# Kernel optimization log

Measured on AMD Instinct MI355X. Metric: run time of the kernel, lower is better.

Reference implementation:

```python
import jax, jax.numpy as jnp
import numpy as np

B, S, D, H, DH, F = 2, 2048, 1024, 16, 64, 4096
EPS = 1e-5


def layernorm(x, gamma, beta):
    mu = jnp.mean(x, axis=-1, keepdims=True)
    var = jnp.mean((x - mu) ** 2, axis=-1, keepdims=True)
    return (x - mu) * jax.lax.rsqrt(var + EPS) * gamma + beta


def setup_inputs() -> dict:
    key = jax.random.key(0)
    ks = jax.random.split(key, 13)
    sc = 0.02
    return {
        "x": jax.random.normal(ks[0], (B, S, D), jnp.float32),
        "W_Q": jax.random.normal(ks[1], (H, DH, D), jnp.float32) * sc,  # per-head [d_head, d_model]
        "W_K": jax.random.normal(ks[2], (H, DH, D), jnp.float32) * sc,
        "W_V": jax.random.normal(ks[3], (H, DH, D), jnp.float32) * sc,
        "W_O": jax.random.normal(ks[4], (H * DH, D), jnp.float32) * sc,
        "W_up": jax.random.normal(ks[5], (D, F), jnp.float32) * sc,
        "b_up": jax.random.normal(ks[6], (F,), jnp.float32) * sc,
        "W_down": jax.random.normal(ks[7], (F, D), jnp.float32) * sc,
        "b_down": jax.random.normal(ks[8], (D,), jnp.float32) * sc,
        "gamma_1": jnp.ones((D,), jnp.float32),
        "beta_1": jnp.zeros((D,), jnp.float32),
        "gamma_2": jnp.ones((D,), jnp.float32),
        "beta_2": jnp.zeros((D,), jnp.float32),
    }


def reference(x, W_Q, W_K, W_V, W_O, W_up, b_up, W_down, b_down, gamma_1, beta_1, gamma_2, beta_2):
    u = layernorm(x, gamma_1, beta_1)
    # per-head projections: input @ W.t() -> [B, H, S, DH]
    Q = jnp.einsum("bsd,hed->bhse", u, W_Q)
    K = jnp.einsum("bsd,hed->bhse", u, W_K)
    V = jnp.einsum("bsd,hed->bhse", u, W_V)
    # Faithful quirk: original does K.reshape(B, DH, S) (raw reshape, NOT transpose)
    K_r = K.reshape(B, H, DH, S)
    scores = jnp.matmul(Q, K_r) / D  # [B,H,S,S]; quirk: scaled by d_model, not sqrt(d_head)
    attn = jax.nn.softmax(scores, axis=-1)
    heads = jnp.matmul(attn, V)  # [B,H,S,DH]
    heads_cat = heads.transpose(0, 2, 1, 3).reshape(B, S, H * DH)  # concat heads on last dim
    z1 = x + heads_cat @ W_O
    v1 = layernorm(z1, gamma_2, beta_2)
    v3 = jax.nn.gelu(v1 @ W_up + b_up, approximate=False)
    z2 = z1 + v3 @ W_down + b_down
    return z2
```

## Files before the change

kernel.cpp:

```cpp
#include <hip/hip_runtime.h>
#include <hip/hip_bf16.h>


typedef __attribute__((ext_vector_type(8))) short short8v;
typedef __attribute__((ext_vector_type(4))) short short4v;
typedef __attribute__((ext_vector_type(4))) float f32x4;

__device__ __forceinline__ float b2f(unsigned short u) {
    unsigned int x = ((unsigned int)u) << 16;
    float f;
    __builtin_memcpy(&f, &x, 4);
    return f;
}
__device__ __forceinline__ unsigned short f2b(float f) {
    unsigned int x;
    __builtin_memcpy(&x, &f, 4);
    unsigned int r = (x + 0x7FFFu + ((x >> 16) & 1u)) >> 16;
    return (unsigned short)r;
}
__device__ __forceinline__ void gload16(const unsigned short* g, unsigned short* l) {
    __builtin_amdgcn_global_load_lds(
        (const __attribute__((address_space(1))) unsigned int*)g,
        (__attribute__((address_space(3))) unsigned int*)l, 16, 0, 0);
}
__device__ __forceinline__ bool is_f32(const unsigned int* flagp) {
    return *flagp == 0x3F800000u;
}

__global__ __launch_bounds__(256) void cast_qkv_k(const void* __restrict__ s0,
                                                  const void* __restrict__ s1,
                                                  const void* __restrict__ s2,
                                                  unsigned short* __restrict__ dst,
                                                  const unsigned int* __restrict__ flagp) {
    const bool f32 = is_f32(flagp);
    const int seg = blockIdx.x >> 9;
    const int i = ((blockIdx.x & 511) * 256 + threadIdx.x) * 8;
    const void* src = seg == 0 ? s0 : (seg == 1 ? s1 : s2);
    unsigned short* d = dst + (size_t)seg * 1048576 + i;
    if (f32) {
        const float* s = (const float*)src + i;
        float4 a = *(const float4*)s;
        float4 b = *(const float4*)(s + 4);
        union { unsigned short u[8]; int4 v; } o;
        o.u[0] = f2b(a.x); o.u[1] = f2b(a.y); o.u[2] = f2b(a.z); o.u[3] = f2b(a.w);
        o.u[4] = f2b(b.x); o.u[5] = f2b(b.y); o.u[6] = f2b(b.z); o.u[7] = f2b(b.w);
        *(int4*)d = o.v;
    } else {
        *(int4*)d = *(const int4*)((const unsigned short*)src + i);
    }
}

__global__ __launch_bounds__(256) void cast_small_k(const void* __restrict__ s0,
                                                    const void* __restrict__ s1,
                                                    const void* __restrict__ s2,
                                                    const void* __restrict__ s3,
                                                    const void* __restrict__ s4,
                                                    const void* __restrict__ s5,
                                                    unsigned short* __restrict__ dst,
                                                    const unsigned int* __restrict__ flagp) {
    const bool f32 = is_f32(flagp);
    const int seg = blockIdx.x < 2 ? 0 : blockIdx.x - 1;
    const void* srcs[6] = {s0, s1, s2, s3, s4, s5};
    const int offs[6] = {0, 4096, 5120, 6144, 7168, 8192};
    const int lens[6] = {4096, 1024, 1024, 1024, 1024, 1024};
    const int base = (blockIdx.x < 2 ? blockIdx.x * 2048 : 0);
    const int i = base + threadIdx.x * 8;
    if (i >= lens[seg]) return;
    const void* src = srcs[seg];
    unsigned short* d = dst + offs[seg] + i;
    if (f32) {
        const float* s = (const float*)src + i;
        float4 a = *(const float4*)s;
        float4 b = *(const float4*)(s + 4);
        union { unsigned short u[8]; int4 v; } o;
        o.u[0] = f2b(a.x); o.u[1] = f2b(a.y); o.u[2] = f2b(a.z); o.u[3] = f2b(a.w);
        o.u[4] = f2b(b.x); o.u[5] = f2b(b.y); o.u[6] = f2b(b.z); o.u[7] = f2b(b.w);
        *(int4*)d = o.v;
    } else {
        *(int4*)d = *(const int4*)((const unsigned short*)src + i);
    }
}

__global__ __launch_bounds__(256) void castT_k(const void* __restrict__ src,
                                               unsigned short* __restrict__ dst,
                                               int rows, int cols,
                                               const unsigned int* __restrict__ flagp) {
    const bool f32 = is_f32(flagp);
    __shared__ float tile[32][33];
    const int t = threadIdx.x, tx = t & 31, ty = t >> 5;
    const int c0 = blockIdx.x * 32, r0 = blockIdx.y * 32;
#pragma unroll
    for (int i = 0; i < 4; i++) {
        int r = r0 + ty + i * 8;
        float v;
        if (f32) v = ((const float*)src)[(size_t)r * cols + c0 + tx];
        else     v = b2f(((const unsigned short*)src)[(size_t)r * cols + c0 + tx]);
        tile[ty + i * 8][tx] = v;
    }
    __syncthreads();
#pragma unroll
    for (int i = 0; i < 4; i++) {
        int c = c0 + ty + i * 8;
        dst[(size_t)c * rows + r0 + tx] = f2b(tile[tx][ty + i * 8]);
    }
}

__global__ __launch_bounds__(256) void kvT_k(const unsigned short* __restrict__ Kn,
                                             const unsigned short* __restrict__ Vn,
                                             unsigned short* __restrict__ Ktt,
                                             unsigned short* __restrict__ Vtt) {
    __shared__ unsigned short tile[64][72];
    const int blk = blockIdx.x;
    const int bh = blk >> 6;
    const int sub = blk & 63;
    const size_t base = (size_t)bh * (2048 * 64);
    const unsigned short* src;
    unsigned short* dst;
    int R, C, r0, c0;
    if (sub < 32) { src = Kn + base; dst = Ktt + base; R = 64;   C = 2048; r0 = 0;              c0 = sub * 64; }
    else          { src = Vn + base; dst = Vtt + base; R = 2048; C = 64;   r0 = (sub - 32) * 64; c0 = 0; }
    const int t = threadIdx.x;
    const int tx = t & 7, ty = t >> 3;
#pragma unroll
    for (int i = 0; i < 2; i++) {
        int r = ty + i * 32;
        union { int4 v; unsigned short u[8]; } ld;
        ld.v = *(const int4*)&src[(size_t)(r0 + r) * C + c0 + tx * 8];
#pragma unroll
        for (int k = 0; k < 8; k++) tile[tx * 8 + k][r] = ld.u[k];
    }
    __syncthreads();
#pragma unroll
    for (int i = 0; i < 2; i++) {
        int c = ty + i * 32;
        union { int4 v; unsigned short u[8]; } stv;
#pragma unroll
        for (int k = 0; k < 8; k++) stv.u[k] = tile[c][tx * 8 + k];
        *(int4*)&dst[(size_t)(c0 + c) * R + r0 + tx * 8] = stv.v;
    }
}

__global__ __launch_bounds__(256) void fin_k(const float* __restrict__ src,
                                             const unsigned short* __restrict__ P0,
                                             const unsigned short* __restrict__ P1,
                                             const unsigned short* __restrict__ P2,
                                             const unsigned short* __restrict__ P3,
                                             void* __restrict__ dst,
                                             const unsigned short* __restrict__ bias,
                                             const unsigned int* __restrict__ flagp) {
    const bool f32 = is_f32(flagp);
    const int i = (blockIdx.x * 256 + threadIdx.x) * 4;
    float4 v = *(const float4*)(src + i);
    uint2 p0 = *(const uint2*)(P0 + i);
    uint2 p1 = *(const uint2*)(P1 + i);
    uint2 p2 = *(const uint2*)(P2 + i);
    uint2 p3 = *(const uint2*)(P3 + i);
    int c = i & 1023;
    v.x += b2f(bias[c])     + b2f((unsigned short)(p0.x & 0xffff)) + b2f((unsigned short)(p1.x & 0xffff))
                            + b2f((unsigned short)(p2.x & 0xffff)) + b2f((unsigned short)(p3.x & 0xffff));
    v.y += b2f(bias[c + 1]) + b2f((unsigned short)(p0.x >> 16))    + b2f((unsigned short)(p1.x >> 16))
                            + b2f((unsigned short)(p2.x >> 16))    + b2f((unsigned short)(p3.x >> 16));
    v.z += b2f(bias[c + 2]) + b2f((unsigned short)(p0.y & 0xffff)) + b2f((unsigned short)(p1.y & 0xffff))
                            + b2f((unsigned short)(p2.y & 0xffff)) + b2f((unsigned short)(p3.y & 0xffff));
    v.w += b2f(bias[c + 3]) + b2f((unsigned short)(p0.y >> 16))    + b2f((unsigned short)(p1.y >> 16))
                            + b2f((unsigned short)(p2.y >> 16))    + b2f((unsigned short)(p3.y >> 16));
    if (f32) {
        *(float4*)((float*)dst + i) = v;
    } else {
        union { unsigned short u[4]; uint2 q; } o;
        o.u[0] = f2b(v.x); o.u[1] = f2b(v.y); o.u[2] = f2b(v.z); o.u[3] = f2b(v.w);
        *(uint2*)((unsigned short*)dst + i) = o.q;
    }
}

template <int MODE>
__global__ __launch_bounds__(256) void ln_k(const void* __restrict__ inp,
                                            unsigned short* __restrict__ outp,
                                            const unsigned short* __restrict__ gamma,
                                            const unsigned short* __restrict__ beta,
                                            const unsigned int* __restrict__ flagp) {
    const int row = blockIdx.x, t = threadIdx.x;
    float xv[4];
    bool f32 = (MODE == 1) ? true : is_f32(flagp);
    if (f32) {
        const float* p = (const float*)inp + (size_t)row * 1024 + t * 4;
        float4 v = *(const float4*)p;
        xv[0] = v.x; xv[1] = v.y; xv[2] = v.z; xv[3] = v.w;
    } else {
        const unsigned short* p = (const unsigned short*)inp + (size_t)row * 1024 + t * 4;
        uint2 v = *(const uint2*)p;
        xv[0] = b2f((unsigned short)(v.x & 0xffff));
        xv[1] = b2f((unsigned short)(v.x >> 16));
        xv[2] = b2f((unsigned short)(v.y & 0xffff));
        xv[3] = b2f((unsigned short)(v.y >> 16));
    }
    float s = xv[0] + xv[1] + xv[2] + xv[3];
    float q = xv[0] * xv[0] + xv[1] * xv[1] + xv[2] * xv[2] + xv[3] * xv[3];
#pragma unroll
    for (int off = 32; off >= 1; off >>= 1) {
        s += __shfl_xor(s, off);
        q += __shfl_xor(q, off);
    }
    __shared__ float ls[8];
    if ((t & 63) == 0) { ls[t >> 6] = s; ls[4 + (t >> 6)] = q; }
    __syncthreads();
    s = ls[0] + ls[1] + ls[2] + ls[3];
    q = ls[4] + ls[5] + ls[6] + ls[7];
    const float mu = s * (1.f / 1024.f);
    const float rs = rsqrtf(q * (1.f / 1024.f) - mu * mu + 1e-5f);
    union { unsigned short u[4]; uint2 v; } o;
#pragma unroll
    for (int i = 0; i < 4; i++) {
        int c = t * 4 + i;
        o.u[i] = f2b((xv[i] - mu) * rs * b2f(gamma[c]) + b2f(beta[c]));
    }
    *(uint2*)(outp + (size_t)row * 1024 + t * 4) = o.v;
}

template <int EPI>
__global__ __launch_bounds__(256) void gemm_k(const unsigned short* __restrict__ A,
                                              const unsigned short* __restrict__ Bm,
                                              unsigned short* __restrict__ C,
                                              unsigned short* __restrict__ C2,
                                              unsigned short* __restrict__ C3,
                                              const unsigned short* __restrict__ bias,
                                              float* __restrict__ outf,
                                              const void* __restrict__ xres,
                                              const unsigned int* __restrict__ flagp,
                                              int N, int ldk, int tilesM, int tilesN,
                                              int kLen) {
    __shared__ unsigned short As[2][128 * 32];
    __shared__ unsigned short Bs[2][128 * 32];
    const int t = threadIdx.x;
    const int w = t >> 6, lane = t & 63, ln = t & 15, quad = (t & 63) >> 4;
    const int wm = w >> 1, wn = w & 1;
    const int bm = blockIdx.x % tilesM;
    const int bn = (blockIdx.x / tilesM) % tilesN;
    const int kc = blockIdx.x / (tilesM * tilesN);
    const int m0 = bm << 7, n0 = bn << 7;
    const int k0 = kc * kLen;
    f32x4 acc[4][4] = {};

    const int srow = lane >> 2;
    const int scol = (lane & 3) << 3;

    const size_t arow[2] = {(size_t)(m0 + (0 * 4 + w) * 16 + srow) * ldk + scol,
                            (size_t)(m0 + (1 * 4 + w) * 16 + srow) * ldk + scol};
    const size_t brow[2] = {(size_t)(n0 + (0 * 4 + w) * 16 + srow) * ldk + scol,
                            (size_t)(n0 + (1 * 4 + w) * 16 + srow) * ldk + scol};

#pragma unroll
    for (int r = 0; r < 2; r++) {
        const int blk = r * 4 + w;
        gload16(&A[arow[r] + k0], &As[0][blk * 512]);
        gload16(&Bm[brow[r] + k0], &Bs[0][blk * 512]);
    }

    int cur = 0;
    for (int kt = k0; kt < k0 + kLen; kt += 32) {
        asm volatile("s_waitcnt vmcnt(0)" ::: "memory");
        __syncthreads();
        if (kt + 32 < k0 + kLen) {
#pragma unroll
            for (int r = 0; r < 2; r++) {
                const int blk = r * 4 + w;
                gload16(&A[arow[r] + kt + 32], &As[cur ^ 1][blk * 512]);
                gload16(&Bm[brow[r] + kt + 32], &Bs[cur ^ 1][blk * 512]);
            }
        }
        short8v af[4], bfv[4];
#pragma unroll
        for (int mi = 0; mi < 4; mi++)
            af[mi] = *(const short8v*)&As[cur][(wm * 64 + mi * 16 + ln) * 32 + quad * 8];
#pragma unroll
        for (int nj = 0; nj < 4; nj++)
            bfv[nj] = *(const short8v*)&Bs[cur][(wn * 64 + nj * 16 + ln) * 32 + quad * 8];
#pragma unroll
        for (int mi = 0; mi < 4; mi++)
#pragma unroll
            for (int nj = 0; nj < 4; nj++)
                acc[mi][nj] = __builtin_amdgcn_mfma_f32_16x16x32_bf16(
                    af[mi], bfv[nj], acc[mi][nj], 0, 0, 0);
        cur ^= 1;
    }

    bool xf32 = false;
    if (EPI == 3) xf32 = is_f32(flagp);

#pragma unroll
    for (int mi = 0; mi < 4; mi++) {
#pragma unroll
        for (int nj = 0; nj < 4; nj++) {
#pragma unroll
            for (int r = 0; r < 4; r++) {
                const int m = m0 + wm * 64 + mi * 16 + quad * 4 + r;
                const int n = n0 + wn * 64 + nj * 16 + ln;
                float v = acc[mi][nj][r];
                if (EPI == 3) {
                    float xv = xf32 ? ((const float*)xres)[(size_t)m * N + n]
                                    : b2f(((const unsigned short*)xres)[(size_t)m * N + n]);
                    outf[(size_t)m * N + n] = v + xv;
                }
            }
        }
    }
}

template <int EPI>
__global__ __launch_bounds__(512, 2) void gemm256_k(const unsigned short* __restrict__ A,
                                                    const unsigned short* __restrict__ Bm,
                                                    unsigned short* __restrict__ C,
                                                    unsigned short* __restrict__ C2,
                                                    unsigned short* __restrict__ C3,
                                                    const unsigned short* __restrict__ bias,
                                                    int N, int ldk, int tilesM, int tilesN,
                                                    int kLen) {
    __shared__ unsigned short As[4][8192];
    __shared__ unsigned short Bs[4][8192];
    const int t = threadIdx.x;
    const int w = t >> 6, l = t & 63, ln = t & 15, quad = (t & 63) >> 4;
    const int wm = w >> 2, wn = w & 3;

    const int nwg = gridDim.x;
    const int wg = ((int)blockIdx.x & 7) * (nwg >> 3) + ((int)blockIdx.x >> 3);

    const int bm = wg % tilesM;
    const int bn = (wg / tilesM) % tilesN;
    const int kc = wg / (tilesM * tilesN);
    const int m0 = bm << 8, n0 = bn << 8;
    const int k0 = kc * kLen;
    const int nk = kLen >> 5;

    const int lrow = l >> 2;
    const int lswz = (((l & 3) ^ (lrow & 3)) << 3);
    const size_t aG0 = (size_t)(m0 + (w << 4) + lrow) * ldk + k0 + lswz;
    const size_t aG1 = aG0 + ((size_t)ldk << 7);
    const size_t bG0 = (size_t)(n0 + (w << 4) + lrow) * ldk + k0 + lswz;
    const size_t bG1 = bG0 + ((size_t)ldk << 7);
    const int ldsLo = w * 512;
    const int ldsHi = 4096 + w * 512;

    const int swz8 = ((quad ^ (ln & 3)) << 3);
    const int raBase = (wm * 128 + ln) * 32 + swz8;
    const int rbBase = (wn * 64 + ln) * 32 + swz8;

    f32x4 acc[8][4] = {};

    gload16(&A[aG0], &As[0][ldsLo]);
    gload16(&Bm[bG0], &Bs[0][ldsLo]);
    gload16(&A[aG1], &As[0][ldsHi]);
    gload16(&Bm[bG1], &Bs[0][ldsHi]);
    if (nk > 1) {
        gload16(&A[aG0 + 32], &As[1][ldsLo]);
        gload16(&Bm[bG0 + 32], &Bs[1][ldsLo]);
        gload16(&A[aG1 + 32], &As[1][ldsHi]);
        gload16(&Bm[bG1 + 32], &Bs[1][ldsHi]);
    }

    for (int tI = 0; tI < nk; ++tI) {
        const int buf = tI & 3;
        if (tI + 1 < nk) {
            asm volatile("s_waitcnt vmcnt(4)" ::: "memory");
        } else {
            asm volatile("s_waitcnt vmcnt(0)" ::: "memory");
        }
        __builtin_amdgcn_s_barrier();
        __builtin_amdgcn_sched_barrier(0);

        const unsigned short* Ab = As[buf];
        const unsigned short* Bb = Bs[buf];
        const int nb = (tI + 2) & 3;
        const size_t ko = (size_t)(tI + 2) << 5;

        if (tI + 2 < nk) {
            gload16(&A[aG0 + ko], &As[nb][ldsLo]);
            gload16(&Bm[bG0 + ko], &Bs[nb][ldsLo]);
            gload16(&A[aG1 + ko], &As[nb][ldsHi]);
            gload16(&Bm[bG1 + ko], &Bs[nb][ldsHi]);
        }
        short8v bf[4], af[8];
#pragma unroll
        for (int nj = 0; nj < 4; nj++) bf[nj] = *(const short8v*)&Bb[rbBase + nj * 512];
#pragma unroll
        for (int mi = 0; mi < 8; mi++) af[mi] = *(const short8v*)&Ab[raBase + mi * 512];
        asm volatile("s_waitcnt lgkmcnt(0)" ::: "memory");
        __builtin_amdgcn_sched_barrier(0);
        __builtin_amdgcn_s_setprio(1);
#pragma unroll
        for (int mi = 0; mi < 8; mi++)
#pragma unroll
            for (int nj = 0; nj < 4; nj++)
                acc[mi][nj] = __builtin_amdgcn_mfma_f32_16x16x32_bf16(
                    af[mi], bf[nj], acc[mi][nj], 0, 0, 0);
        __builtin_amdgcn_s_setprio(0);
    }

    unsigned short* Cp = C;
    if (EPI == 8) Cp = (kc == 0) ? C : (kc == 1) ? (C + 4194304) : (kc == 2) ? C2 : C3;

#pragma unroll
    for (int mi = 0; mi < 8; mi++) {
#pragma unroll
        for (int nj = 0; nj < 4; nj++) {
#pragma unroll
            for (int r = 0; r < 4; r++) {
                const int m = m0 + wm * 128 + mi * 16 + quad * 4 + r;
                const int n = n0 + wn * 64 + nj * 16 + ln;
                float v = acc[mi][nj][r];
                if (EPI == 4) {
                    float x = v + b2f(bias[n]);
                    Cp[(size_t)m * N + n] = f2b(0.5f * x * (1.f + erff(x * 0.70710678118654752f)));
                } else if (EPI == 6) {
                    int b = m >> 11, s = m & 2047;
                    int seg = n >> 10, nn = n & 1023, h = nn >> 6, e = nn & 63;
                    size_t off = ((size_t)(b * 16 + h) * 2048 + s) * 64 + e;
                    if (seg == 0)      C[off]  = f2b(v);
                    else if (seg == 1) C2[off] = f2b(v);
                    else               C3[off] = f2b(v);
                } else {
                    Cp[(size_t)m * N + n] = f2b(v);
                }
            }
        }
    }
}

__global__ __launch_bounds__(512, 4) void attn_k(const unsigned short* __restrict__ Q,
                                                 const unsigned short* __restrict__ Kt,
                                                 const unsigned short* __restrict__ Vt,
                                                 unsigned short* __restrict__ Hd) {
    __shared__ unsigned short Ks[2][2][128 * 32];
    __shared__ unsigned short Vs[2][64 * 128];
    const int t = threadIdx.x;
    const int w = t >> 6, l = t & 63, ln = t & 15, quad = (t & 63) >> 4;
    const int qt = blockIdx.x & 15, bh = blockIdx.x >> 4;
    const int b = bh >> 4, h = bh & 15;
    const int i0 = qt << 7;

    short8v aq[2];
    {
        const unsigned short* qp =
            Q + ((size_t)bh * 2048 + i0 + w * 16 + ln) * 64 + quad * 8;
        aq[0] = *(const short8v*)qp;
        aq[1] = *(const short8v*)(qp + 32);
    }

    const size_t kbase = (size_t)bh * (2048 * 64);
    const size_t vbase = (size_t)bh * (64 * 2048);

    size_t ksrc[2]; int klds[2];
    size_t vsrc[2]; int vlds[2];
#pragma unroll
    for (int r = 0; r < 2; r++) {
        int idx2 = w * 2 + r;
        int ksp = idx2 & 1, J = idx2 >> 1;
        ksrc[r] = (size_t)(J * 16 + (l >> 2)) * 64 + ksp * 32 + (l & 3) * 8;
        klds[r] = ksp * 4096 + J * 512;
        int c = idx2;
        int e = c * 4 + (l >> 4), pp = l & 15;
        int g = (pp & 8) | ((pp & 7) ^ (e & 7));
        vsrc[r] = (size_t)e * 2048 + g * 8;
        vlds[r] = c * 512;
    }

#pragma unroll
    for (int r = 0; r < 2; r++) {
        gload16(Kt + kbase + ksrc[r], &Ks[0][0][0] + klds[r]);
        gload16(Vt + vbase + vsrc[r], &Vs[0][0] + vlds[r]);
    }

    f32x4 O[4] = {};
    float lsum = 0.f;
    int cur = 0;
    const float sc = 9.765625e-4f;

    for (int jt = 0; jt < 16; jt++) {
        asm volatile("s_waitcnt vmcnt(0)" ::: "memory");
        __syncthreads();
        if (jt < 15) {
            const size_t j1 = (size_t)(jt + 1) << 7;
#pragma unroll
            for (int r = 0; r < 2; r++) {
                gload16(Kt + kbase + j1 * 64 + ksrc[r], &Ks[cur ^ 1][0][0] + klds[r]);
                gload16(Vt + vbase + j1 + vsrc[r], &Vs[cur ^ 1][0] + vlds[r]);
            }
        }

        f32x4 S[8] = {};
#pragma unroll
        for (int ks = 0; ks < 2; ks++) {
#pragma unroll
            for (int nj = 0; nj < 8; nj++) {
                short8v bk = *(const short8v*)&Ks[cur][ks][(nj * 16 + ln) * 32 + quad * 8];
                S[nj] = __builtin_amdgcn_mfma_f32_16x16x32_bf16(bk, aq[ks], S[nj], 0, 0, 0);
            }
        }
        short4v pk[8];
#pragma unroll
        for (int nj = 0; nj < 8; nj++) {
            float p0 = __expf(S[nj][0] * sc);
            float p1 = __expf(S[nj][1] * sc);
            float p2 = __expf(S[nj][2] * sc);
            float p3 = __expf(S[nj][3] * sc);
            lsum += (p0 + p1) + (p2 + p3);
            union { unsigned int w2[2]; short4v v; } pu;
            asm("v_cvt_pk_bf16_f32 %0, %1, %2" : "=v"(pu.w2[0]) : "v"(p0), "v"(p1));
            asm("v_cvt_pk_bf16_f32 %0, %1, %2" : "=v"(pu.w2[1]) : "v"(p2), "v"(p3));
            pk[nj] = pu.v;
        }
#pragma unroll
        for (int nj = 0; nj < 8; nj++) {
            int g = 2 * nj + (quad >> 1);
            int pos = (g & 8) | ((g & 7) ^ (ln & 7));
            int off = pos * 8 + (quad & 1) * 4;
#pragma unroll
            for (int ne = 0; ne < 4; ne++) {
                short4v bv = *(const short4v*)&Vs[cur][(ne * 16 + ln) * 128 + off];
                O[ne] = __builtin_amdgcn_mfma_f32_16x16x16bf16_1k(pk[nj], bv, O[ne], 0, 0, 0);
            }
        }
        cur ^= 1;
    }

    lsum += __shfl_xor(lsum, 16);
    lsum += __shfl_xor(lsum, 32);

#pragma unroll
    for (int r = 0; r < 4; r++) {
        float lr = __shfl(lsum, quad * 4 + r);
        float inv = 1.f / lr;
#pragma unroll
        for (int ne = 0; ne < 4; ne++) {
            int i = i0 + w * 16 + quad * 4 + r;
            int e = ne * 16 + ln;
            Hd[((size_t)(b * 2048 + i)) * 1024 + h * 64 + e] = f2b(O[ne][r] * inv);
        }
    }
}

extern "C" void kernel_launch(void* const* d_in, const int* in_sizes, int n_in,
                              void* d_out, int out_size, void* d_ws, size_t ws_size,
                              hipStream_t stream) {
    const unsigned int* flagp = (const unsigned int*)d_in[9];

    unsigned short* p = (unsigned short*)d_ws;
    unsigned short* Wqkv  = p; p += 3145728;
    unsigned short* WOt   = p; p += 1048576;
    unsigned short* Wupt  = p; p += 4194304;
    unsigned short* Wdnt  = p; p += 4194304;
    unsigned short* smallv = p; p += 9216;
    unsigned short* u     = p; p += 4194304;
    unsigned short* Qn    = p; p += 4194304;
    unsigned short* Kn    = p; p += 4194304;
    unsigned short* Vn    = p; p += 4194304;
    unsigned short* Ktt   = p; p += 4194304;
    unsigned short* Vtt   = p; p += 4194304;
    unsigned short* hd    = p; p += 4194304;
    float*          z1    = (float*)p;
    unsigned short* bupc = smallv;
    unsigned short* bdnc = smallv + 4096;
    unsigned short* g1c  = smallv + 5120;
    unsigned short* be1c = smallv + 6144;
    unsigned short* g2c  = smallv + 7168;
    unsigned short* be2c = smallv + 8192;
    unsigned short* v1   = u;
    unsigned short* v3   = Qn;
    unsigned short* Pd0  = Wqkv;
    unsigned short* Pd2  = Vtt;
    unsigned short* Pd3  = hd;

    dim3 blk(256);
    cast_qkv_k<<<1536, blk, 0, stream>>>(d_in[1], d_in[2], d_in[3], Wqkv, flagp);
    castT_k<<<dim3(32, 32),  blk, 0, stream>>>(d_in[4], WOt,  1024, 1024, flagp);
    castT_k<<<dim3(128, 32), blk, 0, stream>>>(d_in[5], Wupt, 1024, 4096, flagp);
    castT_k<<<dim3(32, 128), blk, 0, stream>>>(d_in[7], Wdnt, 4096, 1024, flagp);
    cast_small_k<<<7, blk, 0, stream>>>(d_in[6], d_in[8], d_in[9], d_in[10], d_in[11],
                                        d_in[12], smallv, flagp);

    ln_k<0><<<4096, blk, 0, stream>>>(d_in[0], u, g1c, be1c, flagp);
    gemm256_k<6><<<192, dim3(512), 0, stream>>>(u, Wqkv, Qn, Kn, Vn, nullptr,
                                                3072, 1024, 16, 12, 1024);
    kvT_k<<<2048, blk, 0, stream>>>(Kn, Vn, Ktt, Vtt);
    attn_k<<<512, dim3(512), 0, stream>>>(Qn, Ktt, Vtt, hd);
    gemm_k<3><<<256, blk, 0, stream>>>(hd, WOt, nullptr, nullptr, nullptr, nullptr, z1,
                                       d_in[0], flagp, 1024, 1024, 32, 8, 1024);
    ln_k<1><<<4096, blk, 0, stream>>>(z1, v1, g2c, be2c, flagp);
    gemm256_k<4><<<256, dim3(512), 0, stream>>>(v1, Wupt, v3, nullptr, nullptr, bupc,
                                                4096, 1024, 16, 16, 1024);
    gemm256_k<8><<<256, dim3(512), 0, stream>>>(v3, Wdnt, Pd0, Pd2, Pd3, nullptr,
                                                1024, 4096, 16, 4, 1024);
    fin_k<<<4096, blk, 0, stream>>>(z1, Pd0, Pd0 + 4194304, Pd2, Pd3, d_out, bdnc, flagp);
}
```

Baseline: 426.2 us.

## Add ping-pong pipelined 256x256 GEMM kernel for QKV and up-projection

Adds a new 256x256-tile bf16 GEMM kernel that splits each K-step into four MFMA phases, separated by barriers and raised wave priority. Global-to-LDS loads for the next tile are interleaved between those phases, and workgroup IDs are remapped across groups of eight. The QKV projection and the GELU up-projection now use this kernel in place of the previous 256-tile GEMM. The goal is to overlap memory traffic with matrix math and improve L2 locality, at the cost of heavy register use (launch bounds of 2) and many barriers.

```diff
diff --git a/kernel.cpp b/kernel.cpp
--- a/kernel.cpp
+++ b/kernel.cpp
@@ -425,6 +425,164 @@
     }
 }
 
+template <int EPI>
+__global__ __launch_bounds__(512, 2) void gemm8p_k(const unsigned short* __restrict__ A,
+                                                   const unsigned short* __restrict__ Bm,
+                                                   unsigned short* __restrict__ C,
+                                                   unsigned short* __restrict__ C2,
+                                                   unsigned short* __restrict__ C3,
+                                                   const unsigned short* __restrict__ bias,
+                                                   int N, int ldk, int tilesM, int tilesN,
+                                                   int kLen) {
+    __shared__ unsigned short LA[2][2][8192];
+    __shared__ unsigned short LB[2][2][8192];
+    const int t = threadIdx.x;
+    const int w = t >> 6, l = t & 63, ln = t & 15, quad = (t & 63) >> 4;
+    const int wm = w >> 2, wn = w & 3;
+
+    const int nwg = gridDim.x;
+    const int wg = ((int)blockIdx.x & 7) * (nwg >> 3) + ((int)blockIdx.x >> 3);
+    const int bm = wg % tilesM;
+    const int bn = (wg / tilesM) % tilesN;
+    const int kc = wg / (tilesM * tilesN);
+    const int m0 = bm << 8, n0 = bn << 8;
+    const int k0 = kc * kLen;
+    const int nk = kLen >> 6;
+
+    const int srow = t >> 3;
+    const int schk = (t & 7) ^ (srow & 7);
+    const size_t agb[2] = {(size_t)(m0 + 0 * 128 + srow) * ldk + k0 + schk * 8,
+                           (size_t)(m0 + 1 * 128 + srow) * ldk + k0 + schk * 8};
+    const size_t bgb[2] = {(size_t)(n0 + 0 * 128 + srow) * ldk + k0 + schk * 8,
+                           (size_t)(n0 + 1 * 128 + srow) * ldk + k0 + schk * 8};
+    const size_t rstep = (size_t)ldk << 6;
+    const int wlds = w * 512;
+
+#define STAGE_A(d, h, Tt)                                                     \
+    { const unsigned short* g = &A[agb[h] + ((size_t)(Tt) << 6)];             \
+      unsigned short* p0 = &LA[d][h][wlds];                                   \
+      gload16(g, p0); gload16(g + rstep, p0 + 4096); }
+#define STAGE_B(d, h, Tt)                                                     \
+    { const unsigned short* g = &Bm[bgb[h] + ((size_t)(Tt) << 6)];            \
+      unsigned short* p0 = &LB[d][h][wlds];                                   \
+      gload16(g, p0); gload16(g + rstep, p0 + 4096); }
+
+    const int rslot = ln & 7;
+    const int koff0 = ((quad ^ rslot) << 3);
+    const int koff1 = (((4 | quad) ^ rslot) << 3);
+    const unsigned short* Ard[2] = {&LA[0][wm][ln * 64], &LA[1][wm][ln * 64]};
+    const unsigned short* Brd[2] = {&LB[0][wn >> 1][((wn & 1) * 64 + ln) * 64],
+                                    &LB[1][wn >> 1][((wn & 1) * 64 + ln) * 64]};
+
+    f32x4 acc[8][4] = {};
+    short8v af[4], bf[4];
+
+    STAGE_B(0, 0, 0); STAGE_B(0, 1, 0); STAGE_A(0, 0, 0); STAGE_A(0, 1, 0);
+    if (nk > 1) STAGE_B(1, 0, 1);
+
+    for (int T = 0; T < nk; ++T) {
+        const int d = T & 1;
+        const unsigned short* Ab = Ard[d];
+        const unsigned short* Bb = Brd[d];
+
+        if (T + 1 < nk) {
+            asm volatile("s_waitcnt vmcnt(2)" ::: "memory");
+        } else {
+            asm volatile("s_waitcnt vmcnt(0)" ::: "memory");
+        }
+        if (T + 1 < nk) { STAGE_B(d ^ 1, 1, T + 1); STAGE_A(d ^ 1, 0, T + 1); }
+        __builtin_amdgcn_s_barrier();
+        asm volatile("" ::: "memory");
+        __builtin_amdgcn_sched_barrier(0);
+#pragma unroll
+        for (int nj = 0; nj < 4; nj++) bf[nj] = *(const short8v*)(Bb + nj * 1024 + koff0);
+#pragma unroll
+        for (int q = 0; q < 4; q++) af[q] = *(const short8v*)(Ab + q * 1024 + koff0);
+        asm volatile("s_waitcnt lgkmcnt(0)" ::: "memory");
+        __builtin_amdgcn_sched_barrier(0);
+        __builtin_amdgcn_s_setprio(1);
+#pragma unroll
+        for (int q = 0; q < 4; q++)
+#pragma unroll
+            for (int nj = 0; nj < 4; nj++)
+                acc[q][nj] = __builtin_amdgcn_mfma_f32_16x16x32_bf16(af[q], bf[nj], acc[q][nj], 0, 0, 0);
+        __builtin_amdgcn_s_setprio(0);
+        __builtin_amdgcn_s_barrier();
+
+#pragma unroll
+        for (int q = 0; q < 4; q++) af[q] = *(const short8v*)(Ab + (4 + q) * 1024 + koff0);
+        if (T + 1 < nk) { STAGE_A(d ^ 1, 1, T + 1); }
+        __builtin_amdgcn_s_barrier();
+        asm volatile("s_waitcnt lgkmcnt(0)" ::: "memory");
+        __builtin_amdgcn_sched_barrier(0);
+        __builtin_amdgcn_s_setprio(1);
+#pragma unroll
+        for (int q = 0; q < 4; q++)
+#pragma unroll
+            for (int nj = 0; nj < 4; nj++)
+                acc[4 + q][nj] = __builtin_amdgcn_mfma_f32_16x16x32_bf16(af[q], bf[nj], acc[4 + q][nj], 0, 0, 0);
+        __builtin_amdgcn_s_setprio(0);
+        __builtin_amdgcn_s_barrier();
+
+#pragma unroll
+        for (int nj = 0; nj < 4; nj++) bf[nj] = *(const short8v*)(Bb + nj * 1024 + koff1);
+#pragma unroll
+        for (int q = 0; q < 4; q++) af[q] = *(const short8v*)(Ab + q * 1024 + koff1);
+        __builtin_amdgcn_s_barrier();
+        asm volatile("s_waitcnt lgkmcnt(0)" ::: "memory");
+        __builtin_amdgcn_sched_barrier(0);
+        __builtin_amdgcn_s_setprio(1);
+#pragma unroll
+        for (int q = 0; q < 4; q++)
+#pragma unroll
+            for (int nj = 0; nj < 4; nj++)
+                acc[q][nj] = __builtin_amdgcn_mfma_f32_16x16x32_bf16(af[q], bf[nj], acc[q][nj], 0, 0, 0);
+        __builtin_amdgcn_s_setprio(0);
+        __builtin_amdgcn_s_barrier();
+
+#pragma unroll
+        for (int q = 0; q < 4; q++) af[q] = *(const short8v*)(Ab + (4 + q) * 1024 + koff1);
+        if (T + 2 < nk) { STAGE_B(d, 0, T + 2); }
+        __builtin_amdgcn_s_barrier();
+        asm volatile("s_waitcnt lgkmcnt(0)" ::: "memory");
+        __builtin_amdgcn_sched_barrier(0);
+        __builtin_amdgcn_s_setprio(1);
+#pragma unroll
+        for (int q = 0; q < 4; q++)
+#pragma unroll
+            for (int nj = 0; nj < 4; nj++)
+                acc[4 + q][nj] = __builtin_amdgcn_mfma_f32_16x16x32_bf16(af[q], bf[nj], acc[4 + q][nj], 0, 0, 0);
+        __builtin_amdgcn_s_setprio(0);
+        __builtin_amdgcn_s_barrier();
+    }
+#undef STAGE_A
+#undef STAGE_B
+
+#pragma unroll
+    for (int mi = 0; mi < 8; mi++) {
+#pragma unroll
+        for (int nj = 0; nj < 4; nj++) {
+#pragma unroll
+            for (int r = 0; r < 4; r++) {
+                const int m = m0 + wm * 128 + mi * 16 + quad * 4 + r;
+                const int n = n0 + wn * 64 + nj * 16 + ln;
+                float v = acc[mi][nj][r];
+                if (EPI == 4) {
+                    float x = v + b2f(bias[n]);
+                    C[(size_t)m * N + n] = f2b(0.5f * x * (1.f + erff(x * 0.70710678118654752f)));
+                } else if (EPI == 6) {
+                    int b = m >> 11, s = m & 2047;
+                    int seg = n >> 10, nn = n & 1023, h = nn >> 6, e = nn & 63;
+                    size_t off = ((size_t)(b * 16 + h) * 2048 + s) * 64 + e;
+                    if (seg == 0)      C[off]  = f2b(v);
+                    else if (seg == 1) C2[off] = f2b(v);
+                    else               C3[off] = f2b(v);
+                }
+            }
+        }
+    }
+}
+
 __global__ __launch_bounds__(512, 4) void attn_k(const unsigned short* __restrict__ Q,
                                                  const unsigned short* __restrict__ Kt,
                                                  const unsigned short* __restrict__ Vt,
@@ -578,15 +736,15 @@
                                         d_in[12], smallv, flagp);
 
     ln_k<0><<<4096, blk, 0, stream>>>(d_in[0], u, g1c, be1c, flagp);
-    gemm256_k<6><<<192, dim3(512), 0, stream>>>(u, Wqkv, Qn, Kn, Vn, nullptr,
-                                                3072, 1024, 16, 12, 1024);
+    gemm8p_k<6><<<192, dim3(512), 0, stream>>>(u, Wqkv, Qn, Kn, Vn, nullptr,
+                                               3072, 1024, 16, 12, 1024);
     kvT_k<<<2048, blk, 0, stream>>>(Kn, Vn, Ktt, Vtt);
     attn_k<<<512, dim3(512), 0, stream>>>(Qn, Ktt, Vtt, hd);
     gemm_k<3><<<256, blk, 0, stream>>>(hd, WOt, nullptr, nullptr, nullptr, nullptr, z1,
                                        d_in[0], flagp, 1024, 1024, 32, 8, 1024);
     ln_k<1><<<4096, blk, 0, stream>>>(z1, v1, g2c, be2c, flagp);
-    gemm256_k<4><<<256, dim3(512), 0, stream>>>(v1, Wupt, v3, nullptr, nullptr, bupc,
-                                                4096, 1024, 16, 16, 1024);
+    gemm8p_k<4><<<256, dim3(512), 0, stream>>>(v1, Wupt, v3, nullptr, nullptr, bupc,
+                                               4096, 1024, 16, 16, 1024);
     gemm256_k<8><<<256, dim3(512), 0, stream>>>(v3, Wdnt, Pd0, Pd2, Pd3, nullptr,
                                                 1024, 4096, 16, 4, 1024);
     fin_k<<<4096, blk, 0, stream>>>(z1, Pd0, Pd0 + 4194304, Pd2, Pd3, d_out, bdnc, flagp);
```

Result: slower. 443.8 us (+4.1%).
